# Performance work log

Hardware: AMD Instinct MI355X
Metric: run time of the kernel (lower is better)

Reference implementation:

```python
import jax, jax.numpy as jnp
import numpy as np

N = 50000      # num nodes
E = 800000     # num edges
IN_C = 256
OUT_C = 128


def setup_inputs() -> dict:
    key = jax.random.key(0)
    k1, k2, k3, k4 = jax.random.split(key, 4)
    x = jax.random.normal(k1, (N, IN_C), dtype=jnp.float32)
    edge_index = jax.random.randint(k2, (2, E), 0, N, dtype=jnp.int64)
    # Linear params (Kaiming-uniform-ish scale like torch Linear reset)
    bound = 1.0 / np.sqrt(IN_C)
    W = jax.random.uniform(k3, (OUT_C, IN_C), minval=-bound, maxval=bound, dtype=jnp.float32)
    b = jax.random.uniform(k4, (OUT_C,), minval=-bound, maxval=bound, dtype=jnp.float32)
    return {"x": x, "edge_index": edge_index, "W": W, "b": b}


def reference(x, edge_index, W, b):
    # out = Linear(x): [N, OUT_C]
    out = jnp.einsum("ni,oi->no", x, W) + b
    src, dst = edge_index[0], edge_index[1]
    # gather source features: [E, OUT_C]
    src_feat = out[src]
    # scatter-mean by destination node
    summed = jax.ops.segment_sum(src_feat, dst, num_segments=N)  # [N, OUT_C]
    counts = jax.ops.segment_sum(jnp.ones((E,), dtype=out.dtype), dst, num_segments=N)
    mean = summed / jnp.maximum(counts, 1.0)[:, None]
    return mean
```

## Files before the change

kernel.cpp:

```cpp
#include <hip/hip_runtime.h>

#define N_NODES 50000
#define N_EDGES 800000
#define IN_CH   256
#define OUT_CH  128

#define NB        391
#define CAP       3072
#define L1_CHUNK  2048
#define L1_BLOCKS ((N_EDGES + L1_CHUNK - 1) / L1_CHUNK)

typedef __attribute__((ext_vector_type(8))) short short8;
typedef __attribute__((ext_vector_type(4))) float f32x4;

__device__ __forceinline__ short f2bf(float f) {
    unsigned u = __float_as_uint(f);
    unsigned r = (u + 0x7fffu + ((u >> 16) & 1u)) >> 16;
    return (short)r;
}

__global__ __launch_bounds__(256) void convert_w(const float* __restrict__ W,
                                                 short* __restrict__ Wbf,
                                                 int* __restrict__ bcnt) {
    int t = blockIdx.x * 256 + threadIdx.x;
    const float* wp = W + t * 8;
    float4 v0 = ((const float4*)wp)[0];
    float4 v1 = ((const float4*)wp)[1];
    short8 s;
    s[0]=f2bf(v0.x); s[1]=f2bf(v0.y); s[2]=f2bf(v0.z); s[3]=f2bf(v0.w);
    s[4]=f2bf(v1.x); s[5]=f2bf(v1.y); s[6]=f2bf(v1.z); s[7]=f2bf(v1.w);
    *(short8*)&Wbf[t * 8] = s;
    if (t < NB) bcnt[t] = 0;
}

#define GBM 128
#define GBK 32
#define LDK 40
__global__ __launch_bounds__(256) void gemm_mfma(const float* __restrict__ x,
                                                 const short* __restrict__ Wbf,
                                                 const float* __restrict__ bias,
                                                 short* __restrict__ linbf) {
    __shared__ short As[GBM * LDK];
    __shared__ short Bs[OUT_CH * LDK];

    const int tid = threadIdx.x;
    const int m0  = blockIdx.x * GBM;
    const int w    = tid >> 6;
    const int lane = tid & 63;
    const int lm   = lane & 15;
    const int lq   = lane >> 4;
    const int wrow = (w >> 1) * 64;
    const int wcol = (w & 1) * 64;

    f32x4 acc[4][4];
#pragma unroll
    for (int i = 0; i < 4; ++i)
#pragma unroll
        for (int j = 0; j < 4; ++j) acc[i][j] = (f32x4)(0.0f);

    const int srow  = tid >> 1;
    const int shalf = tid & 1;

    for (int k0 = 0; k0 < IN_CH; k0 += GBK) {
        {
            float4 v0 = make_float4(0.f,0.f,0.f,0.f), v1 = v0, v2 = v0, v3 = v0;
            if (m0 + srow < N_NODES) {
                const float* xp = x + (size_t)(m0 + srow) * IN_CH + k0 + shalf * 16;
                v0 = ((const float4*)xp)[0];
                v1 = ((const float4*)xp)[1];
                v2 = ((const float4*)xp)[2];
                v3 = ((const float4*)xp)[3];
            }
            short8 s0, s1;
            s0[0]=f2bf(v0.x); s0[1]=f2bf(v0.y); s0[2]=f2bf(v0.z); s0[3]=f2bf(v0.w);
            s0[4]=f2bf(v1.x); s0[5]=f2bf(v1.y); s0[6]=f2bf(v1.z); s0[7]=f2bf(v1.w);
            s1[0]=f2bf(v2.x); s1[1]=f2bf(v2.y); s1[2]=f2bf(v2.z); s1[3]=f2bf(v2.w);
            s1[4]=f2bf(v3.x); s1[5]=f2bf(v3.y); s1[6]=f2bf(v3.z); s1[7]=f2bf(v3.w);
            *(short8*)&As[srow * LDK + shalf * 16]     = s0;
            *(short8*)&As[srow * LDK + shalf * 16 + 8] = s1;
        }
        {
            const short* wp = Wbf + (size_t)srow * IN_CH + k0 + shalf * 16;
            *(short8*)&Bs[srow * LDK + shalf * 16]     = ((const short8*)wp)[0];
            *(short8*)&Bs[srow * LDK + shalf * 16 + 8] = ((const short8*)wp)[1];
        }
        __syncthreads();

        short8 af[4], bfr[4];
#pragma unroll
        for (int rt = 0; rt < 4; ++rt)
            af[rt] = *(const short8*)&As[(wrow + rt * 16 + lm) * LDK + lq * 8];
#pragma unroll
        for (int ct = 0; ct < 4; ++ct)
            bfr[ct] = *(const short8*)&Bs[(wcol + ct * 16 + lm) * LDK + lq * 8];
#pragma unroll
        for (int rt = 0; rt < 4; ++rt)
#pragma unroll
            for (int ct = 0; ct < 4; ++ct)
                acc[rt][ct] = __builtin_amdgcn_mfma_f32_16x16x32_bf16(
                    af[rt], bfr[ct], acc[rt][ct], 0, 0, 0);
        __syncthreads();
    }

#pragma unroll
    for (int ct = 0; ct < 4; ++ct) {
        int gcol = wcol + ct * 16 + lm;
        float bv = bias[gcol];
#pragma unroll
        for (int rt = 0; rt < 4; ++rt) {
#pragma unroll
            for (int r = 0; r < 4; ++r) {
                int grow = m0 + wrow + rt * 16 + lq * 4 + r;
                if (grow < N_NODES)
                    linbf[(size_t)grow * OUT_CH + gcol] = f2bf(acc[rt][ct][r] + bv);
            }
        }
    }
}

__global__ __launch_bounds__(256) void bucket_scatter(const int* __restrict__ src,
                                                      const int* __restrict__ dst,
                                                      int* __restrict__ bcnt,
                                                      unsigned* __restrict__ rec) {
    __shared__ int lhist[NB];
    __shared__ int lscan[NB];
    __shared__ int lbase[NB];
    __shared__ unsigned staged[L1_CHUNK];

    const int tid = threadIdx.x;
    const int e0  = blockIdx.x * L1_CHUNK;
    const int total = min(L1_CHUNK, N_EDGES - e0);

    for (int i = tid; i < NB; i += 256) lhist[i] = 0;
    __syncthreads();

    unsigned mypk[8];
    int myr[8];
    int myb[8];
#pragma unroll
    for (int j = 0; j < 8; ++j) {
        int i = tid + j * 256;
        myb[j] = -1;
        if (i < total) {
            unsigned d = (unsigned)dst[e0 + i];
            unsigned s = (unsigned)src[e0 + i];
            int b = (int)(d >> 7);
            myb[j] = b;
            mypk[j] = s | ((d & 127u) << 16) | ((unsigned)b << 23);
            myr[j] = atomicAdd(&lhist[b], 1);
        }
    }
    __syncthreads();

    if (tid < 64) {
        int carry = 0;
        for (int c = 0; c < NB; c += 64) {
            int idx = c + tid;
            int v = (idx < NB) ? lhist[idx] : 0;
            int incl = v;
#pragma unroll
            for (int s = 1; s < 64; s <<= 1) {
                int t = __shfl_up(incl, s, 64);
                if (tid >= s) incl += t;
            }
            if (idx < NB) lscan[idx] = carry + incl - v;
            carry += __shfl(incl, 63, 64);
        }
    }
    __syncthreads();

    for (int bkt = tid; bkt < NB; bkt += 256) {
        int c = lhist[bkt];
        lbase[bkt] = c ? atomicAdd(&bcnt[bkt], c) : 0;
    }
#pragma unroll
    for (int j = 0; j < 8; ++j) {
        if (myb[j] >= 0)
            staged[lscan[myb[j]] + myr[j]] = mypk[j];
    }
    __syncthreads();

    for (int p = tid; p < total; p += 256) {
        unsigned r = staged[p];
        int b = (int)(r >> 23);
        int gpos = lbase[b] + (p - lscan[b]);
        if (gpos < CAP)
            rec[(size_t)b * CAP + gpos] = r;
    }
}

__global__ __launch_bounds__(256) void fine_sort(const int* __restrict__ bcnt,
                                                 const unsigned* __restrict__ rec,
                                                 unsigned short* __restrict__ srcs,
                                                 int* __restrict__ off_g,
                                                 int* __restrict__ deg_g) {
    __shared__ unsigned srec[CAP];
    __shared__ int fh[128], fo[128], fc[128];

    const int b = blockIdx.x;
    const int tid = threadIdx.x;
    const int cnt = min(bcnt[b], CAP);

    for (int i = tid; i < cnt; i += 256)
        srec[i] = rec[(size_t)b * CAP + i];
    if (tid < 128) fh[tid] = 0;
    __syncthreads();

    for (int i = tid; i < cnt; i += 256)
        atomicAdd(&fh[(srec[i] >> 16) & 127u], 1);
    __syncthreads();

    if (tid < 64) {
        int carry = 0;
        for (int c = 0; c < 128; c += 64) {
            int v = fh[c + tid];
            int incl = v;
#pragma unroll
            for (int s = 1; s < 64; s <<= 1) {
                int t = __shfl_up(incl, s, 64);
                if (tid >= s) incl += t;
            }
            fo[c + tid] = carry + incl - v;
            carry += __shfl(incl, 63, 64);
        }
    }
    __syncthreads();

    if (tid < 128) {
        int node = b * 128 + tid;
        if (node < N_NODES) {
            off_g[node] = b * CAP + fo[tid];
            deg_g[node] = fh[tid];
        }
        fc[tid] = fo[tid];
    }
    __syncthreads();

    for (int i = tid; i < cnt; i += 256) {
        unsigned r = srec[i];
        int p = atomicAdd(&fc[(r >> 16) & 127u], 1);
        srcs[(size_t)b * CAP + p] = (unsigned short)(r & 0xffffu);
    }
}

__global__ __launch_bounds__(256) void gather_mean(const unsigned short* __restrict__ srcs,
                                                   const int* __restrict__ off_g,
                                                   const int* __restrict__ deg_g,
                                                   const short* __restrict__ linbf,
                                                   float* __restrict__ out) {
    int n = blockIdx.x * 16 + (threadIdx.x >> 4);
    if (n >= N_NODES) return;
    const int l = threadIdx.x & 15;
    const int beg = off_g[n];
    const int deg = deg_g[n];
    const int end = beg + deg;

    float a[8];
#pragma unroll
    for (int j = 0; j < 8; ++j) a[j] = 0.0f;

    int i = beg;
    for (; i + 3 < end; i += 4) {
        uint4 u[4];
#pragma unroll
        for (int e = 0; e < 4; ++e) {
            int s = srcs[i + e];
            u[e] = *(const uint4*)&linbf[(size_t)s * OUT_CH + l * 8];
        }
#pragma unroll
        for (int e = 0; e < 4; ++e) {
            const unsigned* p = (const unsigned*)&u[e];
#pragma unroll
            for (int j = 0; j < 4; ++j) {
                a[2*j]   += __uint_as_float(p[j] << 16);
                a[2*j+1] += __uint_as_float(p[j] & 0xffff0000u);
            }
        }
    }
    for (; i < end; ++i) {
        int s = srcs[i];
        uint4 u0 = *(const uint4*)&linbf[(size_t)s * OUT_CH + l * 8];
        const unsigned* p0 = (const unsigned*)&u0;
#pragma unroll
        for (int j = 0; j < 4; ++j) {
            a[2*j]   += __uint_as_float(p0[j] << 16);
            a[2*j+1] += __uint_as_float(p0[j] & 0xffff0000u);
        }
    }
    float inv = 1.0f / (float)(deg > 1 ? deg : 1);
    float4 o0, o1;
    o0.x = a[0]*inv; o0.y = a[1]*inv; o0.z = a[2]*inv; o0.w = a[3]*inv;
    o1.x = a[4]*inv; o1.y = a[5]*inv; o1.z = a[6]*inv; o1.w = a[7]*inv;
    float* op = &out[(size_t)n * OUT_CH + l * 8];
    ((float4*)op)[0] = o0;
    ((float4*)op)[1] = o1;
}

extern "C" void kernel_launch(void* const* d_in, const int* in_sizes, int n_in,
                              void* d_out, int out_size, void* d_ws, size_t ws_size,
                              hipStream_t stream) {
    const float* x  = (const float*)d_in[0];
    const int*   ei = (const int*)d_in[1];
    const float* W  = (const float*)d_in[2];
    const float* b  = (const float*)d_in[3];
    float* out = (float*)d_out;

    const int* src = ei;
    const int* dst = ei + N_EDGES;

    char* ws = (char*)d_ws;
    short*    linbf = (short*)ws;    ws += ((size_t)N_NODES * OUT_CH * sizeof(short) + 255) & ~255ull;
    short*    Wbf   = (short*)ws;    ws += ((size_t)IN_CH * OUT_CH * sizeof(short) + 255) & ~255ull;
    unsigned* rec   = (unsigned*)ws; ws += ((size_t)NB * CAP * sizeof(unsigned) + 255) & ~255ull;
    unsigned short* srcs = (unsigned short*)ws;
                                     ws += ((size_t)NB * CAP * sizeof(unsigned short) + 255) & ~255ull;
    int* off_g = (int*)ws;           ws += ((size_t)N_NODES * sizeof(int) + 255) & ~255ull;
    int* deg_g = (int*)ws;           ws += ((size_t)N_NODES * sizeof(int) + 255) & ~255ull;
    int* bcnt  = (int*)ws;

    convert_w<<<16, 256, 0, stream>>>(W, Wbf, bcnt);
    gemm_mfma<<<(N_NODES + GBM - 1) / GBM, 256, 0, stream>>>(x, Wbf, b, linbf);
    bucket_scatter<<<L1_BLOCKS, 256, 0, stream>>>(src, dst, bcnt, rec);
    fine_sort<<<NB, 256, 0, stream>>>(bcnt, rec, srcs, off_g, deg_g);
    gather_mean<<<(N_NODES + 15) / 16, 256, 0, stream>>>(srcs, off_g, deg_g, linbf, out);
}
```

Measured before the change: 163.3 us.

## Fuse GEMM with edge bucketing and fine sort with gather-mean

The GEMM and the edge bucket-scatter become one launch, with blocks split by block index and sharing one reinterpreted shared-memory buffer. The per-bucket fine sort is merged with the gather-mean, so the sorted source list, offsets and degrees stay in LDS instead of round-tripping through global memory. Two launches and the srcs/off/deg global traffic go away. In exchange the gather phase now runs in only 391 blocks that each walk 128 nodes in sequence, which lowers the parallelism available to hide the latency of the random linbf loads.

```diff
diff --git a/kernel.cpp b/kernel.cpp
--- a/kernel.cpp
+++ b/kernel.cpp
@@ -8,7 +8,7 @@
 #define NB        391
 #define CAP       3072
 #define L1_CHUNK  2048
-#define L1_BLOCKS ((N_EDGES + L1_CHUNK - 1) / L1_CHUNK)
+#define NGEMM     ((N_NODES + 127) / 128)
 
 typedef __attribute__((ext_vector_type(8))) short short8;
 typedef __attribute__((ext_vector_type(4))) float f32x4;
@@ -36,165 +36,168 @@
 #define GBM 128
 #define GBK 32
 #define LDK 40
-__global__ __launch_bounds__(256) void gemm_mfma(const float* __restrict__ x,
-                                                 const short* __restrict__ Wbf,
-                                                 const float* __restrict__ bias,
-                                                 short* __restrict__ linbf) {
-    __shared__ short As[GBM * LDK];
-    __shared__ short Bs[OUT_CH * LDK];
-
+__global__ __launch_bounds__(256) void gemm_bucket(const float* __restrict__ x,
+                                                   const short* __restrict__ Wbf,
+                                                   const float* __restrict__ bias,
+                                                   short* __restrict__ linbf,
+                                                   const int* __restrict__ src,
+                                                   const int* __restrict__ dst,
+                                                   int* __restrict__ bcnt,
+                                                   unsigned* __restrict__ rec) {
+    __shared__ __align__(16) char smem[20480];
     const int tid = threadIdx.x;
-    const int m0  = blockIdx.x * GBM;
-    const int w    = tid >> 6;
-    const int lane = tid & 63;
-    const int lm   = lane & 15;
-    const int lq   = lane >> 4;
-    const int wrow = (w >> 1) * 64;
-    const int wcol = (w & 1) * 64;
-
-    f32x4 acc[4][4];
-#pragma unroll
-    for (int i = 0; i < 4; ++i)
-#pragma unroll
-        for (int j = 0; j < 4; ++j) acc[i][j] = (f32x4)(0.0f);
-
-    const int srow  = tid >> 1;
-    const int shalf = tid & 1;
-
-    for (int k0 = 0; k0 < IN_CH; k0 += GBK) {
-        {
-            float4 v0 = make_float4(0.f,0.f,0.f,0.f), v1 = v0, v2 = v0, v3 = v0;
-            if (m0 + srow < N_NODES) {
-                const float* xp = x + (size_t)(m0 + srow) * IN_CH + k0 + shalf * 16;
-                v0 = ((const float4*)xp)[0];
-                v1 = ((const float4*)xp)[1];
-                v2 = ((const float4*)xp)[2];
-                v3 = ((const float4*)xp)[3];
-            }
-            short8 s0, s1;
-            s0[0]=f2bf(v0.x); s0[1]=f2bf(v0.y); s0[2]=f2bf(v0.z); s0[3]=f2bf(v0.w);
-            s0[4]=f2bf(v1.x); s0[5]=f2bf(v1.y); s0[6]=f2bf(v1.z); s0[7]=f2bf(v1.w);
-            s1[0]=f2bf(v2.x); s1[1]=f2bf(v2.y); s1[2]=f2bf(v2.z); s1[3]=f2bf(v2.w);
-            s1[4]=f2bf(v3.x); s1[5]=f2bf(v3.y); s1[6]=f2bf(v3.z); s1[7]=f2bf(v3.w);
-            *(short8*)&As[srow * LDK + shalf * 16]     = s0;
-            *(short8*)&As[srow * LDK + shalf * 16 + 8] = s1;
-        }
-        {
-            const short* wp = Wbf + (size_t)srow * IN_CH + k0 + shalf * 16;
-            *(short8*)&Bs[srow * LDK + shalf * 16]     = ((const short8*)wp)[0];
-            *(short8*)&Bs[srow * LDK + shalf * 16 + 8] = ((const short8*)wp)[1];
-        }
+
+    if (blockIdx.x < NGEMM) {
+        short* As = (short*)smem;
+        short* Bs = (short*)(smem + 10240);
+
+        const int m0  = blockIdx.x * GBM;
+        const int w    = tid >> 6;
+        const int lane = tid & 63;
+        const int lm   = lane & 15;
+        const int lq   = lane >> 4;
+        const int wrow = (w >> 1) * 64;
+        const int wcol = (w & 1) * 64;
+
+        f32x4 acc[4][4];
+#pragma unroll
+        for (int i = 0; i < 4; ++i)
+#pragma unroll
+            for (int j = 0; j < 4; ++j) acc[i][j] = (f32x4)(0.0f);
+
+        const int srow  = tid >> 1;
+        const int shalf = tid & 1;
+
+        for (int k0 = 0; k0 < IN_CH; k0 += GBK) {
+            {
+                float4 v0 = make_float4(0.f,0.f,0.f,0.f), v1 = v0, v2 = v0, v3 = v0;
+                if (m0 + srow < N_NODES) {
+                    const float* xp = x + (size_t)(m0 + srow) * IN_CH + k0 + shalf * 16;
+                    v0 = ((const float4*)xp)[0];
+                    v1 = ((const float4*)xp)[1];
+                    v2 = ((const float4*)xp)[2];
+                    v3 = ((const float4*)xp)[3];
+                }
+                short8 s0, s1;
+                s0[0]=f2bf(v0.x); s0[1]=f2bf(v0.y); s0[2]=f2bf(v0.z); s0[3]=f2bf(v0.w);
+                s0[4]=f2bf(v1.x); s0[5]=f2bf(v1.y); s0[6]=f2bf(v1.z); s0[7]=f2bf(v1.w);
+                s1[0]=f2bf(v2.x); s1[1]=f2bf(v2.y); s1[2]=f2bf(v2.z); s1[3]=f2bf(v2.w);
+                s1[4]=f2bf(v3.x); s1[5]=f2bf(v3.y); s1[6]=f2bf(v3.z); s1[7]=f2bf(v3.w);
+                *(short8*)&As[srow * LDK + shalf * 16]     = s0;
+                *(short8*)&As[srow * LDK + shalf * 16 + 8] = s1;
+            }
+            {
+                const short* wp = Wbf + (size_t)srow * IN_CH + k0 + shalf * 16;
+                *(short8*)&Bs[srow * LDK + shalf * 16]     = ((const short8*)wp)[0];
+                *(short8*)&Bs[srow * LDK + shalf * 16 + 8] = ((const short8*)wp)[1];
+            }
+            __syncthreads();
+
+            short8 af[4], bfr[4];
+#pragma unroll
+            for (int rt = 0; rt < 4; ++rt)
+                af[rt] = *(const short8*)&As[(wrow + rt * 16 + lm) * LDK + lq * 8];
+#pragma unroll
+            for (int ct = 0; ct < 4; ++ct)
+                bfr[ct] = *(const short8*)&Bs[(wcol + ct * 16 + lm) * LDK + lq * 8];
+#pragma unroll
+            for (int rt = 0; rt < 4; ++rt)
+#pragma unroll
+                for (int ct = 0; ct < 4; ++ct)
+                    acc[rt][ct] = __builtin_amdgcn_mfma_f32_16x16x32_bf16(
+                        af[rt], bfr[ct], acc[rt][ct], 0, 0, 0);
+            __syncthreads();
+        }
+
+#pragma unroll
+        for (int ct = 0; ct < 4; ++ct) {
+            int gcol = wcol + ct * 16 + lm;
+            float bv = bias[gcol];
+#pragma unroll
+            for (int rt = 0; rt < 4; ++rt) {
+#pragma unroll
+                for (int r = 0; r < 4; ++r) {
+                    int grow = m0 + wrow + rt * 16 + lq * 4 + r;
+                    if (grow < N_NODES)
+                        linbf[(size_t)grow * OUT_CH + gcol] = f2bf(acc[rt][ct][r] + bv);
+                }
+            }
+        }
+    } else {
+        int* lhist       = (int*)smem;
+        int* lscan       = (int*)(smem + 1568);
+        int* lbase       = (int*)(smem + 3136);
+        unsigned* staged = (unsigned*)(smem + 4704);
+
+        const int blk = blockIdx.x - NGEMM;
+        const int e0  = blk * L1_CHUNK;
+        const int total = min(L1_CHUNK, N_EDGES - e0);
+
+        for (int i = tid; i < NB; i += 256) lhist[i] = 0;
         __syncthreads();
 
-        short8 af[4], bfr[4];
-#pragma unroll
-        for (int rt = 0; rt < 4; ++rt)
-            af[rt] = *(const short8*)&As[(wrow + rt * 16 + lm) * LDK + lq * 8];
-#pragma unroll
-        for (int ct = 0; ct < 4; ++ct)
-            bfr[ct] = *(const short8*)&Bs[(wcol + ct * 16 + lm) * LDK + lq * 8];
-#pragma unroll
-        for (int rt = 0; rt < 4; ++rt)
-#pragma unroll
-            for (int ct = 0; ct < 4; ++ct)
-                acc[rt][ct] = __builtin_amdgcn_mfma_f32_16x16x32_bf16(
-                    af[rt], bfr[ct], acc[rt][ct], 0, 0, 0);
+        unsigned mypk[8];
+        int myr[8];
+        int myb[8];
+#pragma unroll
+        for (int j = 0; j < 8; ++j) {
+            int i = tid + j * 256;
+            myb[j] = -1;
+            if (i < total) {
+                unsigned d = (unsigned)dst[e0 + i];
+                unsigned s = (unsigned)src[e0 + i];
+                int b = (int)(d >> 7);
+                myb[j] = b;
+                mypk[j] = s | ((d & 127u) << 16) | ((unsigned)b << 23);
+                myr[j] = atomicAdd(&lhist[b], 1);
+            }
+        }
         __syncthreads();
+
+        if (tid < 64) {
+            int carry = 0;
+            for (int c = 0; c < NB; c += 64) {
+                int idx = c + tid;
+                int v = (idx < NB) ? lhist[idx] : 0;
+                int incl = v;
+#pragma unroll
+                for (int s = 1; s < 64; s <<= 1) {
+                    int t = __shfl_up(incl, s, 64);
+                    if (tid >= s) incl += t;
+                }
+                if (idx < NB) lscan[idx] = carry + incl - v;
+                carry += __shfl(incl, 63, 64);
+            }
+        }
+        __syncthreads();
+
+        for (int bkt = tid; bkt < NB; bkt += 256) {
+            int c = lhist[bkt];
+            lbase[bkt] = c ? atomicAdd(&bcnt[bkt], c) : 0;
+        }
+#pragma unroll
+        for (int j = 0; j < 8; ++j) {
+            if (myb[j] >= 0)
+                staged[lscan[myb[j]] + myr[j]] = mypk[j];
+        }
+        __syncthreads();
+
+        for (int p = tid; p < total; p += 256) {
+            unsigned r = staged[p];
+            int b = (int)(r >> 23);
+            int gpos = lbase[b] + (p - lscan[b]);
+            if (gpos < CAP)
+                rec[(size_t)b * CAP + gpos] = r;
+        }
     }
-
-#pragma unroll
-    for (int ct = 0; ct < 4; ++ct) {
-        int gcol = wcol + ct * 16 + lm;
-        float bv = bias[gcol];
-#pragma unroll
-        for (int rt = 0; rt < 4; ++rt) {
-#pragma unroll
-            for (int r = 0; r < 4; ++r) {
-                int grow = m0 + wrow + rt * 16 + lq * 4 + r;
-                if (grow < N_NODES)
-                    linbf[(size_t)grow * OUT_CH + gcol] = f2bf(acc[rt][ct][r] + bv);
-            }
-        }
-    }
-}
-
-__global__ __launch_bounds__(256) void bucket_scatter(const int* __restrict__ src,
-                                                      const int* __restrict__ dst,
-                                                      int* __restrict__ bcnt,
-                                                      unsigned* __restrict__ rec) {
-    __shared__ int lhist[NB];
-    __shared__ int lscan[NB];
-    __shared__ int lbase[NB];
-    __shared__ unsigned staged[L1_CHUNK];
-
-    const int tid = threadIdx.x;
-    const int e0  = blockIdx.x * L1_CHUNK;
-    const int total = min(L1_CHUNK, N_EDGES - e0);
-
-    for (int i = tid; i < NB; i += 256) lhist[i] = 0;
-    __syncthreads();
-
-    unsigned mypk[8];
-    int myr[8];
-    int myb[8];
-#pragma unroll
-    for (int j = 0; j < 8; ++j) {
-        int i = tid + j * 256;
-        myb[j] = -1;
-        if (i < total) {
-            unsigned d = (unsigned)dst[e0 + i];
-            unsigned s = (unsigned)src[e0 + i];
-            int b = (int)(d >> 7);
-            myb[j] = b;
-            mypk[j] = s | ((d & 127u) << 16) | ((unsigned)b << 23);
-            myr[j] = atomicAdd(&lhist[b], 1);
-        }
-    }
-    __syncthreads();
-
-    if (tid < 64) {
-        int carry = 0;
-        for (int c = 0; c < NB; c += 64) {
-            int idx = c + tid;
-            int v = (idx < NB) ? lhist[idx] : 0;
-            int incl = v;
-#pragma unroll
-            for (int s = 1; s < 64; s <<= 1) {
-                int t = __shfl_up(incl, s, 64);
-                if (tid >= s) incl += t;
-            }
-            if (idx < NB) lscan[idx] = carry + incl - v;
-            carry += __shfl(incl, 63, 64);
-        }
-    }
-    __syncthreads();
-
-    for (int bkt = tid; bkt < NB; bkt += 256) {
-        int c = lhist[bkt];
-        lbase[bkt] = c ? atomicAdd(&bcnt[bkt], c) : 0;
-    }
-#pragma unroll
-    for (int j = 0; j < 8; ++j) {
-        if (myb[j] >= 0)
-            staged[lscan[myb[j]] + myr[j]] = mypk[j];
-    }
-    __syncthreads();
-
-    for (int p = tid; p < total; p += 256) {
-        unsigned r = staged[p];
-        int b = (int)(r >> 23);
-        int gpos = lbase[b] + (p - lscan[b]);
-        if (gpos < CAP)
-            rec[(size_t)b * CAP + gpos] = r;
-    }
-}
-
-__global__ __launch_bounds__(256) void fine_sort(const int* __restrict__ bcnt,
-                                                 const unsigned* __restrict__ rec,
-                                                 unsigned short* __restrict__ srcs,
-                                                 int* __restrict__ off_g,
-                                                 int* __restrict__ deg_g) {
+}
+
+__global__ __launch_bounds__(256) void fine_gather(const int* __restrict__ bcnt,
+                                                   const unsigned* __restrict__ rec,
+                                                   const short* __restrict__ linbf,
+                                                   float* __restrict__ out) {
     __shared__ unsigned srec[CAP];
+    __shared__ unsigned short ssrc[CAP];
     __shared__ int fh[128], fo[128], fc[128];
 
     const int b = blockIdx.x;
@@ -225,75 +228,66 @@
         }
     }
     __syncthreads();
-
-    if (tid < 128) {
-        int node = b * 128 + tid;
-        if (node < N_NODES) {
-            off_g[node] = b * CAP + fo[tid];
-            deg_g[node] = fh[tid];
-        }
-        fc[tid] = fo[tid];
-    }
+    if (tid < 128) fc[tid] = fo[tid];
     __syncthreads();
 
     for (int i = tid; i < cnt; i += 256) {
         unsigned r = srec[i];
         int p = atomicAdd(&fc[(r >> 16) & 127u], 1);
-        srcs[(size_t)b * CAP + p] = (unsigned short)(r & 0xffffu);
+        ssrc[p] = (unsigned short)(r & 0xffffu);
     }
-}
-
-__global__ __launch_bounds__(256) void gather_mean(const unsigned short* __restrict__ srcs,
-                                                   const int* __restrict__ off_g,
-                                                   const int* __restrict__ deg_g,
-                                                   const short* __restrict__ linbf,
-                                                   float* __restrict__ out) {
-    int n = blockIdx.x * 16 + (threadIdx.x >> 4);
-    if (n >= N_NODES) return;
-    const int l = threadIdx.x & 15;
-    const int beg = off_g[n];
-    const int deg = deg_g[n];
-    const int end = beg + deg;
-
-    float a[8];
-#pragma unroll
-    for (int j = 0; j < 8; ++j) a[j] = 0.0f;
-
-    int i = beg;
-    for (; i + 3 < end; i += 4) {
-        uint4 u[4];
-#pragma unroll
-        for (int e = 0; e < 4; ++e) {
-            int s = srcs[i + e];
-            u[e] = *(const uint4*)&linbf[(size_t)s * OUT_CH + l * 8];
-        }
-#pragma unroll
-        for (int e = 0; e < 4; ++e) {
-            const unsigned* p = (const unsigned*)&u[e];
+    __syncthreads();
+
+    const int l = tid & 15;
+#pragma unroll 1
+    for (int g = 0; g < 8; ++g) {
+        int nl = g * 16 + (tid >> 4);
+        int n = b * 128 + nl;
+        if (n >= N_NODES) continue;
+        const int beg = fo[nl];
+        const int deg = fh[nl];
+        const int end = beg + deg;
+
+        float a[8];
+#pragma unroll
+        for (int j = 0; j < 8; ++j) a[j] = 0.0f;
+
+        int i = beg;
+        for (; i + 3 < end; i += 4) {
+            uint4 u[4];
+#pragma unroll
+            for (int e = 0; e < 4; ++e) {
+                int s = ssrc[i + e];
+                u[e] = *(const uint4*)&linbf[(size_t)s * OUT_CH + l * 8];
+            }
+#pragma unroll
+            for (int e = 0; e < 4; ++e) {
+                const unsigned* p = (const unsigned*)&u[e];
+#pragma unroll
+                for (int j = 0; j < 4; ++j) {
+                    a[2*j]   += __uint_as_float(p[j] << 16);
+                    a[2*j+1] += __uint_as_float(p[j] & 0xffff0000u);
+                }
+            }
+        }
+        for (; i < end; ++i) {
+            int s = ssrc[i];
+            uint4 u0 = *(const uint4*)&linbf[(size_t)s * OUT_CH + l * 8];
+            const unsigned* p0 = (const unsigned*)&u0;
 #pragma unroll
             for (int j = 0; j < 4; ++j) {
-                a[2*j]   += __uint_as_float(p[j] << 16);
-                a[2*j+1] += __uint_as_float(p[j] & 0xffff0000u);
-            }
-        }
+                a[2*j]   += __uint_as_float(p0[j] << 16);
+                a[2*j+1] += __uint_as_float(p0[j] & 0xffff0000u);
+            }
+        }
+        float inv = 1.0f / (float)(deg > 1 ? deg : 1);
+        float4 o0, o1;
+        o0.x = a[0]*inv; o0.y = a[1]*inv; o0.z = a[2]*inv; o0.w = a[3]*inv;
+        o1.x = a[4]*inv; o1.y = a[5]*inv; o1.z = a[6]*inv; o1.w = a[7]*inv;
+        float* op = &out[(size_t)n * OUT_CH + l * 8];
+        ((float4*)op)[0] = o0;
+        ((float4*)op)[1] = o1;
     }
-    for (; i < end; ++i) {
-        int s = srcs[i];
-        uint4 u0 = *(const uint4*)&linbf[(size_t)s * OUT_CH + l * 8];
-        const unsigned* p0 = (const unsigned*)&u0;
-#pragma unroll
-        for (int j = 0; j < 4; ++j) {
-            a[2*j]   += __uint_as_float(p0[j] << 16);
-            a[2*j+1] += __uint_as_float(p0[j] & 0xffff0000u);
-        }
-    }
-    float inv = 1.0f / (float)(deg > 1 ? deg : 1);
-    float4 o0, o1;
-    o0.x = a[0]*inv; o0.y = a[1]*inv; o0.z = a[2]*inv; o0.w = a[3]*inv;
-    o1.x = a[4]*inv; o1.y = a[5]*inv; o1.z = a[6]*inv; o1.w = a[7]*inv;
-    float* op = &out[(size_t)n * OUT_CH + l * 8];
-    ((float4*)op)[0] = o0;
-    ((float4*)op)[1] = o1;
 }
 
 extern "C" void kernel_launch(void* const* d_in, const int* in_sizes, int n_in,
@@ -312,15 +306,9 @@
     short*    linbf = (short*)ws;    ws += ((size_t)N_NODES * OUT_CH * sizeof(short) + 255) & ~255ull;
     short*    Wbf   = (short*)ws;    ws += ((size_t)IN_CH * OUT_CH * sizeof(short) + 255) & ~255ull;
     unsigned* rec   = (unsigned*)ws; ws += ((size_t)NB * CAP * sizeof(unsigned) + 255) & ~255ull;
-    unsigned short* srcs = (unsigned short*)ws;
-                                     ws += ((size_t)NB * CAP * sizeof(unsigned short) + 255) & ~255ull;
-    int* off_g = (int*)ws;           ws += ((size_t)N_NODES * sizeof(int) + 255) & ~255ull;
-    int* deg_g = (int*)ws;           ws += ((size_t)N_NODES * sizeof(int) + 255) & ~255ull;
-    int* bcnt  = (int*)ws;
+    int*      bcnt  = (int*)ws;
 
     convert_w<<<16, 256, 0, stream>>>(W, Wbf, bcnt);
-    gemm_mfma<<<(N_NODES + GBM - 1) / GBM, 256, 0, stream>>>(x, Wbf, b, linbf);
-    bucket_scatter<<<L1_BLOCKS, 256, 0, stream>>>(src, dst, bcnt, rec);
-    fine_sort<<<NB, 256, 0, stream>>>(bcnt, rec, srcs, off_g, deg_g);
-    gather_mean<<<(N_NODES + 15) / 16, 256, 0, stream>>>(srcs, off_g, deg_g, linbf, out);
-}
+    gemm_bucket<<<NGEMM + NB, 256, 0, stream>>>(x, Wbf, b, linbf, src, dst, bcnt, rec);
+    fine_gather<<<NB, 256, 0, stream>>>(bcnt, rec, linbf, out);
+}
```

Result: faster. 156.9 us (-3.9%).
